# Performance work log

Hardware: AMD Instinct MI355X
Metric: run time of the kernel (lower is better)

Reference implementation:

```python
import jax, jax.numpy as jnp
import numpy as np

N_TOKENS = 4096
HIDDEN = 2048
INTER = 1024
N_EXPERTS = 8          # routed experts
ZERO_EXPERTS = 2       # Longcat zero-computation (identity) experts
TOP_K = 2
ROUTED_SCALING = 2.5


def setup_inputs() -> dict:
    key = jax.random.key(0)
    k1, k2, k3, k4 = jax.random.split(key, 4)
    hidden_states = jax.random.normal(k1, (N_TOKENS, HIDDEN), dtype=jnp.float32)
    router_w = jax.random.normal(k2, (N_EXPERTS + ZERO_EXPERTS, HIDDEN), dtype=jnp.float32) * 0.02
    correction_bias = jnp.zeros((N_EXPERTS + ZERO_EXPERTS,), dtype=jnp.float32)
    # torch Linear weight layout [out, in]: gate_up [E, 2I, H], down [E, H, I]
    w_gate_up = jax.random.normal(k3, (N_EXPERTS, 2 * INTER, HIDDEN), dtype=jnp.float32) * 0.02
    w_down = jax.random.normal(k4, (N_EXPERTS, HIDDEN, INTER), dtype=jnp.float32) * 0.02
    return {
        'hidden_states': hidden_states,
        'router_w': router_w,
        'correction_bias': correction_bias,
        'w_gate_up': w_gate_up,
        'w_down': w_down,
    }


def reference(hidden_states, router_w, correction_bias, w_gate_up, w_down):
    x = hidden_states  # [N, H]
    # ---- router gemm (fp32, like dsv3_router_gemm) ----
    logits = jnp.einsum('nh,eh->ne', x.astype(jnp.float32), router_w)  # [N, E+Z]
    scores = jax.nn.sigmoid(logits)
    # biased top-k selection (sglang biased topk, renormalize=False)
    _, topk_idx = jax.lax.top_k(scores + correction_bias[None, :], TOP_K)  # [N, K]
    topk_w = jnp.take_along_axis(scores, topk_idx, axis=1)  # raw sigmoid scores
    # ---- combine weights per expert ----
    onehot = jax.nn.one_hot(topk_idx, N_EXPERTS + ZERO_EXPERTS, dtype=topk_w.dtype)  # [N,K,E+Z]
    combine = jnp.einsum('nke,nk->ne', onehot, topk_w)  # [N, E+Z]
    combine_real = combine[:, :N_EXPERTS]               # [N, E]
    w_zero = combine[:, N_EXPERTS:].sum(axis=-1)        # [N] identity-expert weight
    # ---- expert FFN (silu(gate) * up -> down), dense over experts ----
    gu = jnp.einsum('nh,efh->enf', x, w_gate_up)        # [E, N, 2I]
    gate, up = gu[..., :INTER], gu[..., INTER:]
    h = jax.nn.silu(gate) * up                          # [E, N, I]
    y = jnp.einsum('eni,ehi->enh', h, w_down)           # [E, N, H]
    out = jnp.einsum('enh,ne->nh', y, combine_real.astype(y.dtype))
    out = out + w_zero[:, None].astype(out.dtype) * x   # zero experts = identity
    return out * ROUTED_SCALING
```

## Files before the change

kernel.cpp:

```cpp
#include <hip/hip_runtime.h>
#include <cstdint>
#include <cstddef>

#define N_TOKENS 4096
#define HIDDEN   2048
#define INTER    1024
#define NE       8
#define NE_TOT   10
#define SCALE    2.5f

typedef short v8s __attribute__((ext_vector_type(8)));
typedef float v4f __attribute__((ext_vector_type(4)));

static __device__ inline int imin(int a, int b) { return a < b ? a : b; }

__device__ inline unsigned short f2bf(float f) {
  unsigned int u = __float_as_uint(f);
  u += 0x7fffu + ((u >> 16) & 1u);
  return (unsigned short)(u >> 16);
}

__device__ inline void gld_lds16(const void* g, void* l) {
  __builtin_amdgcn_global_load_lds(
      (const __attribute__((address_space(1))) unsigned int*)g,
      (__attribute__((address_space(3))) unsigned int*)l, 16, 0, 0);
}

__global__ void init_kernel(int* counts) {
  if (threadIdx.x < NE) counts[threadIdx.x] = 0;
}

__global__ __launch_bounds__(256) void cvt_kernel(const float* __restrict__ src,
                                                  unsigned short* __restrict__ dst,
                                                  int n8) {
  int i = blockIdx.x * 256 + threadIdx.x;
  if (i >= n8) return;
  size_t b = (size_t)i * 8;
  float4 a0 = *(const float4*)(src + b);
  float4 a1 = *(const float4*)(src + b + 4);
  union { unsigned short u[8]; uint4 v; } r;
  r.u[0] = f2bf(a0.x); r.u[1] = f2bf(a0.y); r.u[2] = f2bf(a0.z); r.u[3] = f2bf(a0.w);
  r.u[4] = f2bf(a1.x); r.u[5] = f2bf(a1.y); r.u[6] = f2bf(a1.z); r.u[7] = f2bf(a1.w);
  *(uint4*)(dst + b) = r.v;
}

__global__ __launch_bounds__(256, 4) void router_kernel(
    const float* __restrict__ x, const float* __restrict__ rw,
    const float* __restrict__ bias, unsigned short* __restrict__ xb,
    int* __restrict__ counts, int* __restrict__ tok_list,
    float* __restrict__ tok_w, float* __restrict__ out) {
  int tid  = threadIdx.x;
  int lane = tid & 63;
  int wid  = tid >> 6;
  int n    = blockIdx.x * 4 + wid;

  const float* xr = x + (size_t)n * HIDDEN;
  float4 xv[8];
#pragma unroll
  for (int i = 0; i < 8; i++) xv[i] = *(const float4*)(xr + (i * 64 + lane) * 4);

  float acc[NE_TOT];
#pragma unroll
  for (int e = 0; e < NE_TOT; e++) {
    const float* wr = rw + (size_t)e * HIDDEN;
    float a = 0.f;
#pragma unroll
    for (int i = 0; i < 8; i++) {
      float4 w = *(const float4*)(wr + (i * 64 + lane) * 4);
      a += xv[i].x * w.x + xv[i].y * w.y + xv[i].z * w.z + xv[i].w * w.w;
    }
    acc[e] = a;
  }
#pragma unroll
  for (int e = 0; e < NE_TOT; e++) {
    float v = acc[e];
#pragma unroll
    for (int off = 32; off > 0; off >>= 1) v += __shfl_xor(v, off, 64);
    acc[e] = v;
  }

  float sc[NE_TOT], sb[NE_TOT];
#pragma unroll
  for (int e = 0; e < NE_TOT; e++) {
    sc[e] = 1.f / (1.f + expf(-acc[e]));
    sb[e] = sc[e] + bias[e];
  }
  int i1 = 0;
  for (int e = 1; e < NE_TOT; e++) if (sb[e] > sb[i1]) i1 = e;
  int i2 = (i1 == 0) ? 1 : 0;
  for (int e = 0; e < NE_TOT; e++) if (e != i1 && sb[e] > sb[i2]) i2 = e;
  float wzero = 0.f;
  if (i1 >= NE) wzero += sc[i1];
  if (i2 >= NE) wzero += sc[i2];
  if (lane == 0) {
#pragma unroll
    for (int tt = 0; tt < 2; tt++) {
      int idx = tt == 0 ? i1 : i2;
      if (idx < NE) {
        int slot = atomicAdd(&counts[idx], 1);
        tok_list[idx * N_TOKENS + slot] = n;
        tok_w[idx * N_TOKENS + slot]    = SCALE * sc[idx];
      }
    }
  }
  float wz = SCALE * wzero;
#pragma unroll
  for (int i = 0; i < 8; i++) {
    int k = (i * 64 + lane) * 4;
    ushort4 ob;
    ob.x = f2bf(xv[i].x); ob.y = f2bf(xv[i].y);
    ob.z = f2bf(xv[i].z); ob.w = f2bf(xv[i].w);
    *(ushort4*)(xb + (size_t)n * HIDDEN + k) = ob;
    float4 o;
    o.x = wz * xv[i].x; o.y = wz * xv[i].y; o.z = wz * xv[i].z; o.w = wz * xv[i].w;
    *(float4*)(out + (size_t)n * HIDDEN + k) = o;
  }
}

__global__ void offsets_kernel(const int* __restrict__ counts, int* __restrict__ offsets) {
  if (threadIdx.x == 0) {
    int s = 0;
    for (int e = 0; e < NE; e++) { offsets[e] = s; s += counts[e]; }
  }
}


__global__ __launch_bounds__(256, 2) void gateup_kernel(
    const unsigned short* __restrict__ xb, const unsigned short* __restrict__ wgu,
    const int* __restrict__ counts, const int* __restrict__ offsets,
    const int* __restrict__ tok_list, unsigned short* __restrict__ h_buf) {
  int jt = blockIdx.x;
  int mt = blockIdx.y;
  int e  = blockIdx.z;
  int count = counts[e];
  if (mt * 128 >= count) return;

  __shared__ unsigned short As[128 * 32];
  __shared__ unsigned short Bs[128 * 32];

  int tid  = threadIdx.x;
  int lane = tid & 63;
  int wm = (tid >> 7) & 1;
  int wn = (tid >> 6) & 1;

  int row0 = tid >> 2, row1 = row0 + 64;
  int col8 = (((tid & 3) ^ ((tid >> 3) & 3)) * 8);

  const int* tl = tok_list + e * N_TOKENS;
  int t0 = tl[imin(mt * 128 + row0, count - 1)];
  int t1 = tl[imin(mt * 128 + row1, count - 1)];
  const unsigned short* ag0 = xb + (size_t)t0 * HIDDEN + col8;
  const unsigned short* ag1 = xb + (size_t)t1 * HIDDEN + col8;

  int wn0 = row0 >> 6, wi0 = row0 & 63;
  int wn1 = row1 >> 6, wi1 = row1 & 63;
  int br0 = (wi0 < 32) ? (jt * 64 + wn0 * 32 + wi0) : (1024 + jt * 64 + wn0 * 32 + (wi0 - 32));
  int br1 = (wi1 < 32) ? (jt * 64 + wn1 * 32 + wi1) : (1024 + jt * 64 + wn1 * 32 + (wi1 - 32));
  const unsigned short* bbase = wgu + (size_t)e * (2 * INTER) * HIDDEN;
  const unsigned short* bg0 = bbase + (size_t)br0 * HIDDEN + col8;
  const unsigned short* bg1 = bbase + (size_t)br1 * HIDDEN + col8;

  v4f acc[4][4];
#pragma unroll
  for (int i = 0; i < 4; i++)
#pragma unroll
    for (int j = 0; j < 4; j++) acc[i][j] = v4f{0.f, 0.f, 0.f, 0.f};

  int mrow = wm * 64 + (lane & 15);
  int nrow = wn * 64 + (lane & 15);
  int kcol = (((lane >> 4) ^ ((lane >> 1) & 3)) * 8);

  for (int kt = 0; kt < HIDDEN / 32; kt++) {
    __syncthreads();
    gld_lds16(ag0, &As[(size_t)tid * 8]);
    gld_lds16(ag1, &As[2048 + (size_t)tid * 8]);
    gld_lds16(bg0, &Bs[(size_t)tid * 8]);
    gld_lds16(bg1, &Bs[2048 + (size_t)tid * 8]);
    ag0 += 32; ag1 += 32; bg0 += 32; bg1 += 32;
    __syncthreads();
    v8s a[4], b[4];
#pragma unroll
    for (int i = 0; i < 4; i++) a[i] = *(const v8s*)&As[(mrow + i * 16) * 32 + kcol];
#pragma unroll
    for (int j = 0; j < 4; j++) b[j] = *(const v8s*)&Bs[(nrow + j * 16) * 32 + kcol];
#pragma unroll
    for (int i = 0; i < 4; i++)
#pragma unroll
      for (int j = 0; j < 4; j++)
        acc[i][j] = __builtin_amdgcn_mfma_f32_16x16x32_bf16(a[i], b[j], acc[i][j], 0, 0, 0);
  }

  int ocol  = lane & 15;
  int orow4 = (lane >> 4) * 4;
  int hoff  = offsets[e];
#pragma unroll
  for (int i = 0; i < 4; i++) {
#pragma unroll
    for (int r = 0; r < 4; r++) {
      int m = mt * 128 + wm * 64 + i * 16 + orow4 + r;
      if (m < count) {
        unsigned short* hrow = h_buf + (size_t)(hoff + m) * INTER;
#pragma unroll
        for (int j = 0; j < 2; j++) {
          float g = acc[i][j][r];
          float u = acc[i][j + 2][r];
          float hv = (g / (1.f + expf(-g))) * u;
          hrow[jt * 64 + wn * 32 + j * 16 + ocol] = f2bf(hv);
        }
      }
    }
  }
}

__global__ __launch_bounds__(256, 2) void down_kernel(
    const unsigned short* __restrict__ h_buf, const unsigned short* __restrict__ wd,
    const int* __restrict__ counts, const int* __restrict__ offsets,
    const int* __restrict__ tok_list, const float* __restrict__ tok_w,
    float* __restrict__ out) {
  int nt = blockIdx.x;
  int mt = blockIdx.y;
  int e  = blockIdx.z;
  int count = counts[e];
  if (mt * 128 >= count) return;

  __shared__ unsigned short As[128 * 32];
  __shared__ unsigned short Bs[128 * 32];

  int tid  = threadIdx.x;
  int lane = tid & 63;
  int wm = (tid >> 7) & 1;
  int wn = (tid >> 6) & 1;

  int row0 = tid >> 2, row1 = row0 + 64;
  int col8 = (((tid & 3) ^ ((tid >> 3) & 3)) * 8);
  int hoff = offsets[e];

  const unsigned short* ag0 =
      h_buf + (size_t)(hoff + imin(mt * 128 + row0, count - 1)) * INTER + col8;
  const unsigned short* ag1 =
      h_buf + (size_t)(hoff + imin(mt * 128 + row1, count - 1)) * INTER + col8;
  const unsigned short* bbase = wd + (size_t)e * HIDDEN * INTER;
  const unsigned short* bg0 = bbase + (size_t)(nt * 128 + row0) * INTER + col8;
  const unsigned short* bg1 = bbase + (size_t)(nt * 128 + row1) * INTER + col8;

  v4f acc[4][4];
#pragma unroll
  for (int i = 0; i < 4; i++)
#pragma unroll
    for (int j = 0; j < 4; j++) acc[i][j] = v4f{0.f, 0.f, 0.f, 0.f};

  int mrow = wm * 64 + (lane & 15);
  int nrow = wn * 64 + (lane & 15);
  int kcol = (((lane >> 4) ^ ((lane >> 1) & 3)) * 8);

  for (int kt = 0; kt < INTER / 32; kt++) {
    __syncthreads();
    gld_lds16(ag0, &As[(size_t)tid * 8]);
    gld_lds16(ag1, &As[2048 + (size_t)tid * 8]);
    gld_lds16(bg0, &Bs[(size_t)tid * 8]);
    gld_lds16(bg1, &Bs[2048 + (size_t)tid * 8]);
    ag0 += 32; ag1 += 32; bg0 += 32; bg1 += 32;
    __syncthreads();
    v8s a[4], b[4];
#pragma unroll
    for (int i = 0; i < 4; i++) a[i] = *(const v8s*)&As[(mrow + i * 16) * 32 + kcol];
#pragma unroll
    for (int j = 0; j < 4; j++) b[j] = *(const v8s*)&Bs[(nrow + j * 16) * 32 + kcol];
#pragma unroll
    for (int i = 0; i < 4; i++)
#pragma unroll
      for (int j = 0; j < 4; j++)
        acc[i][j] = __builtin_amdgcn_mfma_f32_16x16x32_bf16(a[i], b[j], acc[i][j], 0, 0, 0);
  }

  int ocol  = lane & 15;
  int orow4 = (lane >> 4) * 4;
#pragma unroll
  for (int i = 0; i < 4; i++) {
#pragma unroll
    for (int r = 0; r < 4; r++) {
      int m = mt * 128 + wm * 64 + i * 16 + orow4 + r;
      if (m < count) {
        int tok  = tok_list[e * N_TOKENS + m];
        float w  = tok_w[e * N_TOKENS + m];
        float* orow = out + (size_t)tok * HIDDEN + nt * 128 + wn * 64 + ocol;
#pragma unroll
        for (int j = 0; j < 4; j++) atomicAdd(orow + j * 16, acc[i][j][r] * w);
      }
    }
  }
}

extern "C" void kernel_launch(void* const* d_in, const int* in_sizes, int n_in,
                              void* d_out, int out_size, void* d_ws, size_t ws_size,
                              hipStream_t stream) {
  const float* x   = (const float*)d_in[0];
  const float* rw  = (const float*)d_in[1];
  const float* cb  = (const float*)d_in[2];
  const float* wgu = (const float*)d_in[3];
  const float* wd  = (const float*)d_in[4];
  float* out = (float*)d_out;

  char* ws = (char*)d_ws;
  size_t off = 0;
  auto alloc = [&](size_t bytes) {
    void* p = ws + off;
    off += (bytes + 255) & ~(size_t)255;
    return p;
  };
  unsigned short* xb    = (unsigned short*)alloc((size_t)N_TOKENS * HIDDEN * 2);
  unsigned short* wgu_b = (unsigned short*)alloc((size_t)NE * 2 * INTER * HIDDEN * 2);
  unsigned short* wd_b  = (unsigned short*)alloc((size_t)NE * HIDDEN * INTER * 2);
  unsigned short* h_buf = (unsigned short*)alloc((size_t)2 * N_TOKENS * INTER * 2);
  int*   tok_list = (int*)alloc((size_t)NE * N_TOKENS * 4);
  float* tok_w    = (float*)alloc((size_t)NE * N_TOKENS * 4);
  int*   counts   = (int*)alloc(256);
  int*   offsets  = (int*)alloc(256);
  (void)ws_size; (void)in_sizes; (void)n_in; (void)out_size;

  init_kernel<<<1, 64, 0, stream>>>(counts);
  cvt_kernel<<<(NE * 2 * INTER * HIDDEN / 8 + 255) / 256, 256, 0, stream>>>(
      wgu, wgu_b, NE * 2 * INTER * HIDDEN / 8);
  cvt_kernel<<<(NE * HIDDEN * INTER / 8 + 255) / 256, 256, 0, stream>>>(
      wd, wd_b, NE * HIDDEN * INTER / 8);
  router_kernel<<<N_TOKENS / 4, 256, 0, stream>>>(x, rw, cb, xb, counts, tok_list, tok_w, out);
  offsets_kernel<<<1, 64, 0, stream>>>(counts, offsets);
  gateup_kernel<<<dim3(16, 32, 8), 256, 0, stream>>>(xb, wgu_b, counts, offsets, tok_list, h_buf);
  down_kernel<<<dim3(16, 32, 8), 256, 0, stream>>>(h_buf, wd_b, counts, offsets, tok_list, tok_w, out);
}
```

Baseline: 522.0 us.

## Double-buffer LDS tiles in gate-up and down GEMM kernels

Both expert GEMM kernels now keep two LDS buffers for the A and B tiles. The first tile is loaded before the loop, and each iteration issues the asynchronous global-to-LDS loads for the next K tile before running MFMAs on the current one. This hides global load latency behind compute and leaves one barrier per iteration instead of two. In exchange, LDS use per block doubles, and the overlap is limited because the barrier at the end of each iteration still waits for the outstanding loads.

```diff
diff --git a/kernel.cpp b/kernel.cpp
--- a/kernel.cpp
+++ b/kernel.cpp
@@ -135,8 +135,8 @@
   int count = counts[e];
   if (mt * 128 >= count) return;
 
-  __shared__ unsigned short As[128 * 32];
-  __shared__ unsigned short Bs[128 * 32];
+  __shared__ unsigned short As[2][128 * 32];
+  __shared__ unsigned short Bs[2][128 * 32];
 
   int tid  = threadIdx.x;
   int lane = tid & 63;
@@ -170,24 +170,35 @@
   int nrow = wn * 64 + (lane & 15);
   int kcol = (((lane >> 4) ^ ((lane >> 1) & 3)) * 8);
 
-  for (int kt = 0; kt < HIDDEN / 32; kt++) {
-    __syncthreads();
-    gld_lds16(ag0, &As[(size_t)tid * 8]);
-    gld_lds16(ag1, &As[2048 + (size_t)tid * 8]);
-    gld_lds16(bg0, &Bs[(size_t)tid * 8]);
-    gld_lds16(bg1, &Bs[2048 + (size_t)tid * 8]);
-    ag0 += 32; ag1 += 32; bg0 += 32; bg1 += 32;
-    __syncthreads();
+  gld_lds16(ag0, &As[0][(size_t)tid * 8]);
+  gld_lds16(ag1, &As[0][2048 + (size_t)tid * 8]);
+  gld_lds16(bg0, &Bs[0][(size_t)tid * 8]);
+  gld_lds16(bg1, &Bs[0][2048 + (size_t)tid * 8]);
+  ag0 += 32; ag1 += 32; bg0 += 32; bg1 += 32;
+  __syncthreads();
+
+  const int NK = HIDDEN / 32;
+  for (int kt = 0; kt < NK; kt++) {
+    int cur = kt & 1;
+    if (kt + 1 < NK) {
+      int nxt = cur ^ 1;
+      gld_lds16(ag0, &As[nxt][(size_t)tid * 8]);
+      gld_lds16(ag1, &As[nxt][2048 + (size_t)tid * 8]);
+      gld_lds16(bg0, &Bs[nxt][(size_t)tid * 8]);
+      gld_lds16(bg1, &Bs[nxt][2048 + (size_t)tid * 8]);
+      ag0 += 32; ag1 += 32; bg0 += 32; bg1 += 32;
+    }
     v8s a[4], b[4];
 #pragma unroll
-    for (int i = 0; i < 4; i++) a[i] = *(const v8s*)&As[(mrow + i * 16) * 32 + kcol];
-#pragma unroll
-    for (int j = 0; j < 4; j++) b[j] = *(const v8s*)&Bs[(nrow + j * 16) * 32 + kcol];
+    for (int i = 0; i < 4; i++) a[i] = *(const v8s*)&As[cur][(mrow + i * 16) * 32 + kcol];
+#pragma unroll
+    for (int j = 0; j < 4; j++) b[j] = *(const v8s*)&Bs[cur][(nrow + j * 16) * 32 + kcol];
 #pragma unroll
     for (int i = 0; i < 4; i++)
 #pragma unroll
       for (int j = 0; j < 4; j++)
         acc[i][j] = __builtin_amdgcn_mfma_f32_16x16x32_bf16(a[i], b[j], acc[i][j], 0, 0, 0);
+    __syncthreads();
   }
 
   int ocol  = lane & 15;
@@ -223,8 +234,8 @@
   int count = counts[e];
   if (mt * 128 >= count) return;
 
-  __shared__ unsigned short As[128 * 32];
-  __shared__ unsigned short Bs[128 * 32];
+  __shared__ unsigned short As[2][128 * 32];
+  __shared__ unsigned short Bs[2][128 * 32];
 
   int tid  = threadIdx.x;
   int lane = tid & 63;
@@ -253,24 +264,35 @@
   int nrow = wn * 64 + (lane & 15);
   int kcol = (((lane >> 4) ^ ((lane >> 1) & 3)) * 8);
 
-  for (int kt = 0; kt < INTER / 32; kt++) {
-    __syncthreads();
-    gld_lds16(ag0, &As[(size_t)tid * 8]);
-    gld_lds16(ag1, &As[2048 + (size_t)tid * 8]);
-    gld_lds16(bg0, &Bs[(size_t)tid * 8]);
-    gld_lds16(bg1, &Bs[2048 + (size_t)tid * 8]);
-    ag0 += 32; ag1 += 32; bg0 += 32; bg1 += 32;
-    __syncthreads();
+  gld_lds16(ag0, &As[0][(size_t)tid * 8]);
+  gld_lds16(ag1, &As[0][2048 + (size_t)tid * 8]);
+  gld_lds16(bg0, &Bs[0][(size_t)tid * 8]);
+  gld_lds16(bg1, &Bs[0][2048 + (size_t)tid * 8]);
+  ag0 += 32; ag1 += 32; bg0 += 32; bg1 += 32;
+  __syncthreads();
+
+  const int NK = INTER / 32;
+  for (int kt = 0; kt < NK; kt++) {
+    int cur = kt & 1;
+    if (kt + 1 < NK) {
+      int nxt = cur ^ 1;
+      gld_lds16(ag0, &As[nxt][(size_t)tid * 8]);
+      gld_lds16(ag1, &As[nxt][2048 + (size_t)tid * 8]);
+      gld_lds16(bg0, &Bs[nxt][(size_t)tid * 8]);
+      gld_lds16(bg1, &Bs[nxt][2048 + (size_t)tid * 8]);
+      ag0 += 32; ag1 += 32; bg0 += 32; bg1 += 32;
+    }
     v8s a[4], b[4];
 #pragma unroll
-    for (int i = 0; i < 4; i++) a[i] = *(const v8s*)&As[(mrow + i * 16) * 32 + kcol];
-#pragma unroll
-    for (int j = 0; j < 4; j++) b[j] = *(const v8s*)&Bs[(nrow + j * 16) * 32 + kcol];
+    for (int i = 0; i < 4; i++) a[i] = *(const v8s*)&As[cur][(mrow + i * 16) * 32 + kcol];
+#pragma unroll
+    for (int j = 0; j < 4; j++) b[j] = *(const v8s*)&Bs[cur][(nrow + j * 16) * 32 + kcol];
 #pragma unroll
     for (int i = 0; i < 4; i++)
 #pragma unroll
       for (int j = 0; j < 4; j++)
         acc[i][j] = __builtin_amdgcn_mfma_f32_16x16x32_bf16(a[i], b[j], acc[i][j], 0, 0, 0);
+    __syncthreads();
   }
 
   int ocol  = lane & 15;
```

After: 522.8 us. About the same (+0.2%).

## Triple-buffer LDS tiles with async global-to-LDS prefetch in expert GEMMs

Applied to the files above, without the earlier changes.

Replaces the single-buffered load-then-compute loop in the gate-up and down GEMM kernels with a three-stage LDS ring. Tiles for k+1 and k+2 stay in flight via global_load_lds, with explicit vmcnt waits and raw barriers. The goal is to hide global memory latency behind MFMA work instead of stalling on each tile. This triples LDS use per block to 48KB and raises the launch-bounds occupancy hint to 3. The hand-written waitcnt and barrier logic could be fragile.

```diff
diff --git a/kernel.cpp b/kernel.cpp
--- a/kernel.cpp
+++ b/kernel.cpp
@@ -25,6 +25,11 @@
       (const __attribute__((address_space(1))) unsigned int*)g,
       (__attribute__((address_space(3))) unsigned int*)l, 16, 0, 0);
 }
+
+#define FENCE() __asm__ __volatile__("" ::: "memory")
+#define BAR()   do { FENCE(); __builtin_amdgcn_s_barrier(); FENCE(); } while (0)
+#define WAITVM(n) __asm__ __volatile__("s_waitcnt vmcnt(" #n ")" ::: "memory")
+#define WAITLGKM0() __asm__ __volatile__("s_waitcnt lgkmcnt(0)" ::: "memory")
 
 __global__ void init_kernel(int* counts) {
   if (threadIdx.x < NE) counts[threadIdx.x] = 0;
@@ -125,7 +130,7 @@
 }
 
 
-__global__ __launch_bounds__(256, 2) void gateup_kernel(
+__global__ __launch_bounds__(256, 3) void gateup_kernel(
     const unsigned short* __restrict__ xb, const unsigned short* __restrict__ wgu,
     const int* __restrict__ counts, const int* __restrict__ offsets,
     const int* __restrict__ tok_list, unsigned short* __restrict__ h_buf) {
@@ -135,8 +140,8 @@
   int count = counts[e];
   if (mt * 128 >= count) return;
 
-  __shared__ unsigned short As[128 * 32];
-  __shared__ unsigned short Bs[128 * 32];
+  __shared__ unsigned short As[3][128 * 32];
+  __shared__ unsigned short Bs[3][128 * 32];
 
   int tid  = threadIdx.x;
   int lane = tid & 63;
@@ -160,6 +165,14 @@
   const unsigned short* bg0 = bbase + (size_t)br0 * HIDDEN + col8;
   const unsigned short* bg1 = bbase + (size_t)br1 * HIDDEN + col8;
 
+  auto STAGE = [&](int b) {
+    gld_lds16(ag0, &As[b][(size_t)tid * 8]);
+    gld_lds16(ag1, &As[b][2048 + (size_t)tid * 8]);
+    gld_lds16(bg0, &Bs[b][(size_t)tid * 8]);
+    gld_lds16(bg1, &Bs[b][2048 + (size_t)tid * 8]);
+    ag0 += 32; ag1 += 32; bg0 += 32; bg1 += 32;
+  };
+
   v4f acc[4][4];
 #pragma unroll
   for (int i = 0; i < 4; i++)
@@ -170,24 +183,29 @@
   int nrow = wn * 64 + (lane & 15);
   int kcol = (((lane >> 4) ^ ((lane >> 1) & 3)) * 8);
 
-  for (int kt = 0; kt < HIDDEN / 32; kt++) {
-    __syncthreads();
-    gld_lds16(ag0, &As[(size_t)tid * 8]);
-    gld_lds16(ag1, &As[2048 + (size_t)tid * 8]);
-    gld_lds16(bg0, &Bs[(size_t)tid * 8]);
-    gld_lds16(bg1, &Bs[2048 + (size_t)tid * 8]);
-    ag0 += 32; ag1 += 32; bg0 += 32; bg1 += 32;
-    __syncthreads();
+  STAGE(0); STAGE(1); STAGE(2);
+  WAITVM(8);
+  BAR();
+
+  const int NK = HIDDEN / 32;
+  for (int kt = 0; kt < NK; kt++) {
+    int cur = kt % 3;
     v8s a[4], b[4];
 #pragma unroll
-    for (int i = 0; i < 4; i++) a[i] = *(const v8s*)&As[(mrow + i * 16) * 32 + kcol];
-#pragma unroll
-    for (int j = 0; j < 4; j++) b[j] = *(const v8s*)&Bs[(nrow + j * 16) * 32 + kcol];
+    for (int i = 0; i < 4; i++) a[i] = *(const v8s*)&As[cur][(mrow + i * 16) * 32 + kcol];
+#pragma unroll
+    for (int j = 0; j < 4; j++) b[j] = *(const v8s*)&Bs[cur][(nrow + j * 16) * 32 + kcol];
 #pragma unroll
     for (int i = 0; i < 4; i++)
 #pragma unroll
       for (int j = 0; j < 4; j++)
         acc[i][j] = __builtin_amdgcn_mfma_f32_16x16x32_bf16(a[i], b[j], acc[i][j], 0, 0, 0);
+    WAITLGKM0();
+    BAR();
+    if (kt + 3 < NK)      { STAGE(cur); WAITVM(8); }
+    else if (kt + 3 == NK){ WAITVM(4); }
+    else if (kt + 1 < NK) { WAITVM(0); }
+    if (kt + 1 < NK) BAR();
   }
 
   int ocol  = lane & 15;
@@ -212,7 +230,7 @@
   }
 }
 
-__global__ __launch_bounds__(256, 2) void down_kernel(
+__global__ __launch_bounds__(256, 3) void down_kernel(
     const unsigned short* __restrict__ h_buf, const unsigned short* __restrict__ wd,
     const int* __restrict__ counts, const int* __restrict__ offsets,
     const int* __restrict__ tok_list, const float* __restrict__ tok_w,
@@ -223,8 +241,8 @@
   int count = counts[e];
   if (mt * 128 >= count) return;
 
-  __shared__ unsigned short As[128 * 32];
-  __shared__ unsigned short Bs[128 * 32];
+  __shared__ unsigned short As[3][128 * 32];
+  __shared__ unsigned short Bs[3][128 * 32];
 
   int tid  = threadIdx.x;
   int lane = tid & 63;
@@ -243,6 +261,14 @@
   const unsigned short* bg0 = bbase + (size_t)(nt * 128 + row0) * INTER + col8;
   const unsigned short* bg1 = bbase + (size_t)(nt * 128 + row1) * INTER + col8;
 
+  auto STAGE = [&](int b) {
+    gld_lds16(ag0, &As[b][(size_t)tid * 8]);
+    gld_lds16(ag1, &As[b][2048 + (size_t)tid * 8]);
+    gld_lds16(bg0, &Bs[b][(size_t)tid * 8]);
+    gld_lds16(bg1, &Bs[b][2048 + (size_t)tid * 8]);
+    ag0 += 32; ag1 += 32; bg0 += 32; bg1 += 32;
+  };
+
   v4f acc[4][4];
 #pragma unroll
   for (int i = 0; i < 4; i++)
@@ -253,24 +279,29 @@
   int nrow = wn * 64 + (lane & 15);
   int kcol = (((lane >> 4) ^ ((lane >> 1) & 3)) * 8);
 
-  for (int kt = 0; kt < INTER / 32; kt++) {
-    __syncthreads();
-    gld_lds16(ag0, &As[(size_t)tid * 8]);
-    gld_lds16(ag1, &As[2048 + (size_t)tid * 8]);
-    gld_lds16(bg0, &Bs[(size_t)tid * 8]);
-    gld_lds16(bg1, &Bs[2048 + (size_t)tid * 8]);
-    ag0 += 32; ag1 += 32; bg0 += 32; bg1 += 32;
-    __syncthreads();
+  STAGE(0); STAGE(1); STAGE(2);
+  WAITVM(8);
+  BAR();
+
+  const int NK = INTER / 32;
+  for (int kt = 0; kt < NK; kt++) {
+    int cur = kt % 3;
     v8s a[4], b[4];
 #pragma unroll
-    for (int i = 0; i < 4; i++) a[i] = *(const v8s*)&As[(mrow + i * 16) * 32 + kcol];
-#pragma unroll
-    for (int j = 0; j < 4; j++) b[j] = *(const v8s*)&Bs[(nrow + j * 16) * 32 + kcol];
+    for (int i = 0; i < 4; i++) a[i] = *(const v8s*)&As[cur][(mrow + i * 16) * 32 + kcol];
+#pragma unroll
+    for (int j = 0; j < 4; j++) b[j] = *(const v8s*)&Bs[cur][(nrow + j * 16) * 32 + kcol];
 #pragma unroll
     for (int i = 0; i < 4; i++)
 #pragma unroll
       for (int j = 0; j < 4; j++)
         acc[i][j] = __builtin_amdgcn_mfma_f32_16x16x32_bf16(a[i], b[j], acc[i][j], 0, 0, 0);
+    WAITLGKM0();
+    BAR();
+    if (kt + 3 < NK)      { STAGE(cur); WAITVM(8); }
+    else if (kt + 3 == NK){ WAITVM(4); }
+    else if (kt + 1 < NK) { WAITVM(0); }
+    if (kt + 1 < NK) BAR();
   }
 
   int ocol  = lane & 15;
```

Measured after the change: 549.3 us. 1.05x slower.
